# Kernel tuning notes

Hardware: AMD Instinct MI355X
Metric: run time of the kernel (lower is better)

Reference implementation:

```python
import jax, jax.numpy as jnp
import numpy as np

B, C_IN, C_OUT, N, E = 1, 64, 64, 100000, 3200000
BN_EPS = 1e-5


def setup_inputs() -> dict:
    key = jax.random.key(0)
    ks = jax.random.split(key, 8)
    return {
        "in_features": jax.random.normal(ks[0], (B, C_IN, N), dtype=jnp.float32),
        "w_v": jax.random.normal(ks[1], (C_OUT, C_IN), dtype=jnp.float32) * (1.0 / np.sqrt(C_IN)),
        "w_n": jax.random.normal(ks[2], (C_OUT, C_IN), dtype=jnp.float32) * (1.0 / np.sqrt(C_IN)),
        "gamma": jnp.ones((C_OUT,), dtype=jnp.float32),
        "beta": jnp.zeros((C_OUT,), dtype=jnp.float32),
        "prelu_a": jnp.full((1,), 0.25, dtype=jnp.float32),
        "reduce_index": jax.random.randint(ks[3], (E,), 0, N, dtype=jnp.int32),
        "gather_index": jax.random.randint(ks[4], (E,), 0, N, dtype=jnp.int32),
    }


def reference(in_features, w_v, w_n, gamma, beta, prelu_a, reduce_index, gather_index):
    # 1x1 convs == per-node linear maps: [B, C_in, N] -> [B, C_out, N]
    F_v = jnp.einsum('oi,bin->bon', w_v, in_features)
    F_n = jnp.einsum('oi,bin->bon', w_n, in_features)

    # gather source-node features per edge: [E, B, C_out]
    src = jnp.moveaxis(F_n[:, :, gather_index], 2, 0)
    # scatter-mean into destination nodes (include_self=False -> 0 for isolated nodes)
    sums = jax.ops.segment_sum(src, reduce_index, num_segments=N)  # [N, B, C]
    counts = jax.ops.segment_sum(jnp.ones((src.shape[0],), src.dtype), reduce_index,
                                 num_segments=N)  # [N]
    mean = sums / jnp.maximum(counts, 1.0)[:, None, None]  # nodes w/o edges stay 0
    out = jnp.moveaxis(mean, 0, 2) + F_v  # [B, C, N]

    # BatchNorm1d (training mode: biased batch stats over (B, N))
    mu = jnp.mean(out, axis=(0, 2), keepdims=True)
    var = jnp.mean((out - mu) ** 2, axis=(0, 2), keepdims=True)
    out = (out - mu) * jax.lax.rsqrt(var + BN_EPS)
    out = out * gamma[None, :, None] + beta[None, :, None]

    # PReLU with a single shared learnable slope
    out = jnp.where(out >= 0, out, prelu_a[0] * out)
    return out
```

## Files before the change

kernel.cpp:

```cpp
#include <hip/hip_runtime.h>
#include <hip/hip_bf16.h>

#define NODES 100000
#define BN_EPS 1e-5f
#define NB2 256
#define NPB2 391
#define CAP 13072
#define EPB 2048

__device__ __forceinline__ unsigned bf16rne(float f) {
    unsigned u = __float_as_uint(f);
    u += 0x7FFFu + ((u >> 16) & 1u);
    return u >> 16;
}
__device__ __forceinline__ float bflo(unsigned u) { return __uint_as_float(u << 16); }
__device__ __forceinline__ float bfhi(unsigned u) { return __uint_as_float(u & 0xFFFF0000u); }

__global__ __launch_bounds__(256, 8) void k_place(
        const int* __restrict__ ridx, const int* __restrict__ gidx,
        int* __restrict__ cursor, unsigned* __restrict__ packed, int E) {
    __shared__ int lh[4][NB2];
    const int t = threadIdx.x;
    const int w = t >> 6;
    for (int k = t; k < 4 * NB2; k += 256) ((int*)lh)[k] = 0;
    __syncthreads();
    const int base = blockIdx.x * EPB;
    int r[EPB / 256], g[EPB / 256];
#pragma unroll
    for (int k = 0; k < EPB / 256; ++k) {
        int e = base + t + (k << 8);
        r[k] = (e < E) ? ridx[e] : -1;
        g[k] = (e < E) ? gidx[e] : 0;
    }
#pragma unroll
    for (int k = 0; k < EPB / 256; ++k)
        if (r[k] >= 0) atomicAdd(&lh[w][(unsigned)r[k] / NPB2], 1);
    __syncthreads();
    {
        int c0 = lh[0][t], c1 = lh[1][t], c2 = lh[2][t], c3 = lh[3][t];
        int tot = c0 + c1 + c2 + c3;
        if (tot) {
            int g0 = t * CAP + atomicAdd(&cursor[t], tot);
            lh[0][t] = g0;
            lh[1][t] = g0 + c0;
            lh[2][t] = g0 + c0 + c1;
            lh[3][t] = g0 + c0 + c1 + c2;
        }
    }
    __syncthreads();
#pragma unroll
    for (int k = 0; k < EPB / 256; ++k) {
        if (r[k] >= 0) {
            unsigned rr = (unsigned)r[k];
            unsigned b = rr / NPB2;
            int off = atomicAdd(&lh[w][b], 1);
            if (off < (int)((b + 1) * CAP))
                packed[off] = ((rr - b * NPB2) << 17) | (unsigned)g[k];
        }
    }
}

__global__ __launch_bounds__(1024) void k_sortb(
        const int* __restrict__ cursor, unsigned* __restrict__ packed,
        int* __restrict__ nodestart, int* __restrict__ cnt) {
    __shared__ int lh[1024];
    __shared__ int lsc[1024];
    const int b = blockIdx.x, t = threadIdx.x;
    const int s0b = b * CAP;
    int cntb = cursor[b];
    if (cntb > CAP) cntb = CAP;
    unsigned r[(CAP + 1023) / 1024];
#pragma unroll
    for (int kk = 0; kk < (CAP + 1023) / 1024; ++kk) {
        int k = t + kk * 1024;
        if (k < cntb) r[kk] = packed[s0b + k];
    }
    lh[t] = 0;
    __syncthreads();
#pragma unroll
    for (int kk = 0; kk < (CAP + 1023) / 1024; ++kk) {
        int k = t + kk * 1024;
        if (k < cntb) atomicAdd(&lh[r[kk] >> 17], 1);
    }
    __syncthreads();
    lsc[t] = lh[t];
    __syncthreads();
    for (int off = 1; off < 1024; off <<= 1) {
        int v = lsc[t];
        int add = (t >= off) ? lsc[t - off] : 0;
        __syncthreads();
        lsc[t] = v + add;
        __syncthreads();
    }
    int excl = (t == 0) ? 0 : lsc[t - 1];
    if (t < NPB2) {
        int n = b * NPB2 + t;
        if (n < NODES) {
            nodestart[n] = s0b + excl;
            cnt[n] = lh[t];
        }
    }
    __syncthreads();
    lh[t] = excl;
    __syncthreads();
#pragma unroll
    for (int kk = 0; kk < (CAP + 1023) / 1024; ++kk) {
        int k = t + kk * 1024;
        if (k < cntb) {
            unsigned v = r[kk];
            int pos = atomicAdd(&lh[v >> 17], 1);
            packed[s0b + pos] = v & 0x1FFFFu;
        }
    }
}

__global__ __launch_bounds__(256, 4) void k_gemm_bf16(
        const float* __restrict__ x, const float* __restrict__ wn,
        unsigned* __restrict__ Fnh2) {
    __shared__ float lx[64 * 68];
    __shared__ float wt[64 * 68];
    const int t = threadIdx.x;
    const int n0 = blockIdx.x * 64;
    for (int idx = t; idx < 1024; idx += 256) {
        int rr = idx >> 4;
        int q4 = (idx & 15) * 4;
        int n = n0 + q4;
        float4 xv = {0.f, 0.f, 0.f, 0.f};
        if (n < NODES) xv = *(const float4*)(x + rr * NODES + n);
        *(float4*)&lx[rr * 68 + q4] = xv;
        float4 w4 = *(const float4*)(wn + (idx << 2));
        wt[(q4 + 0) * 68 + rr] = w4.x;
        wt[(q4 + 1) * 68 + rr] = w4.y;
        wt[(q4 + 2) * 68 + rr] = w4.z;
        wt[(q4 + 3) * 68 + rr] = w4.w;
    }
    __syncthreads();
    const int c4 = (t & 15) * 4;
    const int j4 = (t >> 4) * 4;
    float4 a0 = {0,0,0,0}, a1 = {0,0,0,0}, a2 = {0,0,0,0}, a3 = {0,0,0,0};
#pragma unroll 8
    for (int ci = 0; ci < 64; ++ci) {
        float4 w = *(const float4*)&wt[ci * 68 + c4];
        float4 xv = *(const float4*)&lx[ci * 68 + j4];
        a0.x += w.x * xv.x; a0.y += w.x * xv.y; a0.z += w.x * xv.z; a0.w += w.x * xv.w;
        a1.x += w.y * xv.x; a1.y += w.y * xv.y; a1.z += w.y * xv.z; a1.w += w.y * xv.w;
        a2.x += w.z * xv.x; a2.y += w.z * xv.y; a2.z += w.z * xv.z; a2.w += w.z * xv.w;
        a3.x += w.w * xv.x; a3.y += w.w * xv.y; a3.z += w.w * xv.z; a3.w += w.w * xv.w;
    }
    uint2* F2 = (uint2*)Fnh2;
#pragma unroll
    for (int k = 0; k < 4; ++k) {
        int n = n0 + j4 + k;
        if (n < NODES) {
            float v0 = (k == 0) ? a0.x : (k == 1) ? a0.y : (k == 2) ? a0.z : a0.w;
            float v1 = (k == 0) ? a1.x : (k == 1) ? a1.y : (k == 2) ? a1.z : a1.w;
            float v2 = (k == 0) ? a2.x : (k == 1) ? a2.y : (k == 2) ? a2.z : a2.w;
            float v3 = (k == 0) ? a3.x : (k == 1) ? a3.y : (k == 2) ? a3.z : a3.w;
            uint2 val;
            val.x = bf16rne(v0) | (bf16rne(v1) << 16);
            val.y = bf16rne(v2) | (bf16rne(v3) << 16);
            F2[n * 16 + (c4 >> 2)] = val;
        }
    }
}

__global__ __launch_bounds__(256) void k_gemm_n(
        const float* __restrict__ x, const float* __restrict__ wn,
        float* __restrict__ Fn) {
    __shared__ float lx[64][65];
    __shared__ float lw[64][65];
    const int t = threadIdx.x;
    const int n0 = blockIdx.x * 64;
    for (int idx = t; idx < 4096; idx += 256) {
        int r = idx >> 6, q = idx & 63;
        lw[r][q] = wn[idx];
        int n = n0 + q;
        lx[r][q] = (n < NODES) ? x[r * NODES + n] : 0.f;
    }
    __syncthreads();
    const int c = t & 63;
    const int jb = t >> 6;
    for (int k = 0; k < 16; ++k) {
        int j = jb + 4 * k;
        int n = n0 + j;
        if (n >= NODES) continue;
        float acc = 0.f;
#pragma unroll
        for (int ci = 0; ci < 64; ++ci)
            acc += lw[c][ci] * lx[ci][j];
        Fn[n * 64 + c] = acc;
    }
}

__global__ __launch_bounds__(256) void k_segreduce(
        const unsigned* __restrict__ Fnh2, const unsigned* __restrict__ packed,
        const int* __restrict__ nodestart, const int* __restrict__ cnt,
        float4* __restrict__ mean4) {
    const int n = (int)((blockIdx.x * 256u + threadIdx.x) >> 6);
    if (n >= NODES) return;
    const int lane = threadIdx.x & 63;
    const int sub = lane >> 3;
    const int cp  = lane & 7;
    const int s0 = nodestart[n];
    const int cn = cnt[n];
    const int s1 = s0 + cn;
    float f0 = 0.f, f1 = 0.f, f2 = 0.f, f3 = 0.f;
    float f4 = 0.f, f5 = 0.f, f6 = 0.f, f7 = 0.f;
    int i = s0;
    for (; i + 15 < s1; i += 16) {
        int ga = (int)packed[i + sub];
        int gb = (int)packed[i + 8 + sub];
        uint4 ua = *(const uint4*)(Fnh2 + (((size_t)ga) << 5) + (cp << 2));
        uint4 ub = *(const uint4*)(Fnh2 + (((size_t)gb) << 5) + (cp << 2));
        f0 += bflo(ua.x) + bflo(ub.x);
        f1 += bfhi(ua.x) + bfhi(ub.x);
        f2 += bflo(ua.y) + bflo(ub.y);
        f3 += bfhi(ua.y) + bfhi(ub.y);
        f4 += bflo(ua.z) + bflo(ub.z);
        f5 += bfhi(ua.z) + bfhi(ub.z);
        f6 += bflo(ua.w) + bflo(ub.w);
        f7 += bfhi(ua.w) + bfhi(ub.w);
    }
    for (; i < s1; i += 8) {
        uint4 u = {0u, 0u, 0u, 0u};
        if (i + sub < s1) {
            int g = (int)packed[i + sub];
            u = *(const uint4*)(Fnh2 + (((size_t)g) << 5) + (cp << 2));
        }
        f0 += bflo(u.x); f1 += bfhi(u.x);
        f2 += bflo(u.y); f3 += bfhi(u.y);
        f4 += bflo(u.z); f5 += bfhi(u.z);
        f6 += bflo(u.w); f7 += bfhi(u.w);
    }
#pragma unroll
    for (int m = 8; m < 64; m <<= 1) {
        f0 += __shfl_xor(f0, m);
        f1 += __shfl_xor(f1, m);
        f2 += __shfl_xor(f2, m);
        f3 += __shfl_xor(f3, m);
        f4 += __shfl_xor(f4, m);
        f5 += __shfl_xor(f5, m);
        f6 += __shfl_xor(f6, m);
        f7 += __shfl_xor(f7, m);
    }
    if (sub == 0) {
        float inv = 1.f / fmaxf((float)cn, 1.f);
        float4 lo4, hi4;
        lo4.x = f0 * inv; lo4.y = f1 * inv; lo4.z = f2 * inv; lo4.w = f3 * inv;
        hi4.x = f4 * inv; hi4.y = f5 * inv; hi4.z = f6 * inv; hi4.w = f7 * inv;
        mean4[n * 16 + cp * 2]     = lo4;
        mean4[n * 16 + cp * 2 + 1] = hi4;
    }
}

__global__ __launch_bounds__(256, 8) void k_combine(
        const float* __restrict__ x, const float* __restrict__ wv,
        const float* __restrict__ sums, const int* __restrict__ counts,
        const int divide,
        float* __restrict__ outpre, float* __restrict__ bn) {
    __shared__ float wt[64 * 68];
    __shared__ float reds[64][5];
    __shared__ float redq[64][5];
    const int t = threadIdx.x;
    const int n0 = blockIdx.x * 64;
    for (int idx = t; idx < 1024; idx += 256) {
        int rr = idx & 63;
        int q4 = (idx >> 6) * 4;
        float4 w4 = *(const float4*)(wv + rr * 64 + q4);
        wt[(q4 + 0) * 68 + rr] = w4.x;
        wt[(q4 + 1) * 68 + rr] = w4.y;
        wt[(q4 + 2) * 68 + rr] = w4.z;
        wt[(q4 + 3) * 68 + rr] = w4.w;
    }
    __syncthreads();
    const int c4 = (t & 15) * 4;
    const int j4 = (t >> 4) * 4;
    const int jn = n0 + j4;
    const bool valid = (jn < NODES);
    const int jc = valid ? jn : 0;
    float4 a0 = {0,0,0,0}, a1 = {0,0,0,0}, a2 = {0,0,0,0}, a3 = {0,0,0,0};
#pragma unroll 4
    for (int ci = 0; ci < 64; ++ci) {
        float4 w = *(const float4*)&wt[ci * 68 + c4];
        float4 xv = *(const float4*)(x + (size_t)ci * NODES + jc);
        a0.x += w.x * xv.x; a0.y += w.x * xv.y; a0.z += w.x * xv.z; a0.w += w.x * xv.w;
        a1.x += w.y * xv.x; a1.y += w.y * xv.y; a1.z += w.y * xv.z; a1.w += w.y * xv.w;
        a2.x += w.z * xv.x; a2.y += w.z * xv.y; a2.z += w.z * xv.z; a2.w += w.z * xv.w;
        a3.x += w.w * xv.x; a3.y += w.w * xv.y; a3.z += w.w * xv.z; a3.w += w.w * xv.w;
    }
    const float4* sums4 = (const float4*)sums;
    float4 mv0 = {0,0,0,0}, mv1 = {0,0,0,0}, mv2 = {0,0,0,0}, mv3 = {0,0,0,0};
    if (valid) {
        mv0 = sums4[(jn + 0) * 16 + (c4 >> 2)];
        mv1 = sums4[(jn + 1) * 16 + (c4 >> 2)];
        mv2 = sums4[(jn + 2) * 16 + (c4 >> 2)];
        mv3 = sums4[(jn + 3) * 16 + (c4 >> 2)];
        if (divide) {
            float i0 = 1.f / fmaxf((float)counts[jn + 0], 1.f);
            float i1 = 1.f / fmaxf((float)counts[jn + 1], 1.f);
            float i2 = 1.f / fmaxf((float)counts[jn + 2], 1.f);
            float i3 = 1.f / fmaxf((float)counts[jn + 3], 1.f);
            mv0.x *= i0; mv0.y *= i0; mv0.z *= i0; mv0.w *= i0;
            mv1.x *= i1; mv1.y *= i1; mv1.z *= i1; mv1.w *= i1;
            mv2.x *= i2; mv2.y *= i2; mv2.z *= i2; mv2.w *= i2;
            mv3.x *= i3; mv3.y *= i3; mv3.z *= i3; mv3.w *= i3;
        }
    }
    float4 st0 = {0,0,0,0}, st1 = {0,0,0,0}, st2 = {0,0,0,0}, st3 = {0,0,0,0};
    if (valid) {
        st0.x = mv0.x + a0.x; st0.y = mv1.x + a0.y; st0.z = mv2.x + a0.z; st0.w = mv3.x + a0.w;
        st1.x = mv0.y + a1.x; st1.y = mv1.y + a1.y; st1.z = mv2.y + a1.z; st1.w = mv3.y + a1.w;
        st2.x = mv0.z + a2.x; st2.y = mv1.z + a2.y; st2.z = mv2.z + a2.z; st2.w = mv3.z + a2.w;
        st3.x = mv0.w + a3.x; st3.y = mv1.w + a3.y; st3.z = mv2.w + a3.z; st3.w = mv3.w + a3.w;
        *(float4*)(outpre + (size_t)(c4 + 0) * NODES + jn) = st0;
        *(float4*)(outpre + (size_t)(c4 + 1) * NODES + jn) = st1;
        *(float4*)(outpre + (size_t)(c4 + 2) * NODES + jn) = st2;
        *(float4*)(outpre + (size_t)(c4 + 3) * NODES + jn) = st3;
    }
    float ls0 = st0.x + st0.y + st0.z + st0.w;
    float ls1 = st1.x + st1.y + st1.z + st1.w;
    float ls2 = st2.x + st2.y + st2.z + st2.w;
    float ls3 = st3.x + st3.y + st3.z + st3.w;
    float lq0 = st0.x*st0.x + st0.y*st0.y + st0.z*st0.z + st0.w*st0.w;
    float lq1 = st1.x*st1.x + st1.y*st1.y + st1.z*st1.z + st1.w*st1.w;
    float lq2 = st2.x*st2.x + st2.y*st2.y + st2.z*st2.z + st2.w*st2.w;
    float lq3 = st3.x*st3.x + st3.y*st3.y + st3.z*st3.z + st3.w*st3.w;
    const int lane = t & 63;
    const int wid = t >> 6;
#pragma unroll
    for (int m = 16; m < 64; m <<= 1) {
        ls0 += __shfl_xor(ls0, m); lq0 += __shfl_xor(lq0, m);
        ls1 += __shfl_xor(ls1, m); lq1 += __shfl_xor(lq1, m);
        ls2 += __shfl_xor(ls2, m); lq2 += __shfl_xor(lq2, m);
        ls3 += __shfl_xor(ls3, m); lq3 += __shfl_xor(lq3, m);
    }
    if (lane < 16) {
        reds[lane * 4 + 0][wid] = ls0; redq[lane * 4 + 0][wid] = lq0;
        reds[lane * 4 + 1][wid] = ls1; redq[lane * 4 + 1][wid] = lq1;
        reds[lane * 4 + 2][wid] = ls2; redq[lane * 4 + 2][wid] = lq2;
        reds[lane * 4 + 3][wid] = ls3; redq[lane * 4 + 3][wid] = lq3;
    }
    __syncthreads();
    if (t < 64) {
        float s = reds[t][0] + reds[t][1] + reds[t][2] + reds[t][3];
        float q = redq[t][0] + redq[t][1] + redq[t][2] + redq[t][3];
        atomicAdd(&bn[t], s);
        atomicAdd(&bn[64 + t], q);
    }
}

__global__ __launch_bounds__(256) void k_final(
        float* __restrict__ out, const float* __restrict__ bn,
        const float* __restrict__ gamma, const float* __restrict__ beta,
        const float* __restrict__ pa) {
    const int c = blockIdx.y;
    const int n = blockIdx.x * 256 + threadIdx.x;
    const float invN = 1.f / (float)NODES;
    float mu = bn[c] * invN;
    float var = fmaxf(bn[64 + c] * invN - mu * mu, 0.f);
    float scale = gamma[c] * rsqrtf(var + BN_EPS);
    float shift = beta[c] - mu * scale;
    float a = pa[0];
    if (n < NODES) {
        float y = out[c * NODES + n] * scale + shift;
        y = (y >= 0.f) ? y : a * y;
        out[c * NODES + n] = y;
    }
}

__global__ __launch_bounds__(256) void k_scatter(
        const float* __restrict__ Fn,
        const int* __restrict__ gidx, const int* __restrict__ ridx,
        float* __restrict__ sums, int* __restrict__ counts, int E) {
    const int wave = (int)((blockIdx.x * blockDim.x + threadIdx.x) >> 6);
    const int lane = threadIdx.x & 63;
    const int base = wave * 64;
    if (base >= E) return;
    const int nvalid = min(64, E - base);
    int g = 0, r = 0;
    if (lane < nvalid) {
        g = gidx[base + lane];
        r = ridx[base + lane];
        atomicAdd(&counts[r], 1);
    }
    for (int i = 0; i < nvalid; ++i) {
        int gg = __shfl(g, i);
        int rr = __shfl(r, i);
        float v = Fn[gg * 64 + lane];
        atomicAdd(&sums[rr * 64 + lane], v);
    }
}

extern "C" void kernel_launch(void* const* d_in, const int* in_sizes, int n_in,
                              void* d_out, int out_size, void* d_ws, size_t ws_size,
                              hipStream_t stream) {
    const float* x     = (const float*)d_in[0];
    const float* w_v   = (const float*)d_in[1];
    const float* w_n   = (const float*)d_in[2];
    const float* gamma = (const float*)d_in[3];
    const float* beta  = (const float*)d_in[4];
    const float* pa    = (const float*)d_in[5];
    const int* ridx    = (const int*)d_in[6];
    const int* gidx    = (const int*)d_in[7];
    float* out = (float*)d_out;

    const int E = in_sizes[6];
    const long long N64 = (long long)NODES * 64;
    const int ntiles = (NODES + 63) / 64;
    const dim3 g4((NODES + 255) / 256, 64);

    size_t need = ((size_t)N64 + (size_t)NB2 * CAP + NB2 + 128
                   + NODES + NODES) * 4;

    if (ws_size >= need) {
        float*    mean      = (float*)d_ws;
        unsigned* packed    = (unsigned*)(mean + N64);
        int*      cursor    = (int*)(packed + (size_t)NB2 * CAP);
        float*    bn        = (float*)(cursor + NB2);
        int*      nodestart = (int*)(bn + 128);
        int*      cntarr    = nodestart + NODES;
        unsigned* Fnh2 = (unsigned*)out;

        hipMemsetAsync(cursor, 0, (NB2 + 128) * sizeof(int), stream);
        k_place<<<(E + EPB - 1) / EPB, 256, 0, stream>>>(ridx, gidx, cursor,
                                                         packed, E);
        k_gemm_bf16<<<ntiles, 256, 0, stream>>>(x, w_n, Fnh2);
        k_sortb<<<NB2, 1024, 0, stream>>>(cursor, packed, nodestart, cntarr);
        k_segreduce<<<(NODES * 64 + 255) / 256, 256, 0, stream>>>(
            Fnh2, packed, nodestart, cntarr, (float4*)mean);
        k_combine<<<ntiles, 256, 0, stream>>>(x, w_v, mean, cntarr, 0, out, bn);
        k_final<<<g4, 256, 0, stream>>>(out, bn, gamma, beta, pa);
    } else {
        float* sums   = (float*)d_ws;
        int*   counts = (int*)(sums + N64);
        float* bn     = (float*)(sums + N64 + NODES);
        float* Fn = out;

        hipMemsetAsync(sums, 0, (size_t)(N64 + NODES + 128) * sizeof(float),
                       stream);
        k_gemm_n<<<ntiles, 256, 0, stream>>>(x, w_n, Fn);
        k_scatter<<<(E + 255) / 256, 256, 0, stream>>>(Fn, gidx, ridx, sums,
                                                       counts, E);
        k_combine<<<ntiles, 256, 0, stream>>>(x, w_v, sums, counts, 1, out, bn);
        k_final<<<g4, 256, 0, stream>>>(out, bn, gamma, beta, pa);
    }
}
```

Measured before the change: 300.5 us.

## Retile node GEMMs over channel blocks and store mean in channel-blocked layout

```diff
diff --git a/kernel.cpp b/kernel.cpp
--- a/kernel.cpp
+++ b/kernel.cpp
@@ -114,52 +114,58 @@
     }
 }
 
-__global__ __launch_bounds__(256, 4) void k_gemm_bf16(
+__global__ __launch_bounds__(256, 3) void k_gemm_bf16_2(
         const float* __restrict__ x, const float* __restrict__ wn,
         unsigned* __restrict__ Fnh2) {
-    __shared__ float lx[64 * 68];
-    __shared__ float wt[64 * 68];
+    __shared__ float wt[64 * 16];
     const int t = threadIdx.x;
-    const int n0 = blockIdx.x * 64;
+    const int cb = blockIdx.y;
+    const int c0 = cb * 16;
     for (int idx = t; idx < 1024; idx += 256) {
-        int rr = idx >> 4;
-        int q4 = (idx & 15) * 4;
-        int n = n0 + q4;
-        float4 xv = {0.f, 0.f, 0.f, 0.f};
-        if (n < NODES) xv = *(const float4*)(x + rr * NODES + n);
-        *(float4*)&lx[rr * 68 + q4] = xv;
-        float4 w4 = *(const float4*)(wn + (idx << 2));
-        wt[(q4 + 0) * 68 + rr] = w4.x;
-        wt[(q4 + 1) * 68 + rr] = w4.y;
-        wt[(q4 + 2) * 68 + rr] = w4.z;
-        wt[(q4 + 3) * 68 + rr] = w4.w;
-    }
-    __syncthreads();
-    const int c4 = (t & 15) * 4;
-    const int j4 = (t >> 4) * 4;
-    float4 a0 = {0,0,0,0}, a1 = {0,0,0,0}, a2 = {0,0,0,0}, a3 = {0,0,0,0};
-#pragma unroll 8
+        int ci = idx >> 4, co = idx & 15;
+        wt[ci * 16 + co] = wn[(c0 + co) * 64 + ci];
+    }
+    __syncthreads();
+    const int j4 = (blockIdx.x * 256 + t) * 4;
+    const bool valid = (j4 < NODES);
+    const int jc = valid ? j4 : 0;
+    float4 acc[16];
+#pragma unroll
+    for (int q = 0; q < 16; ++q) acc[q] = {0.f, 0.f, 0.f, 0.f};
+#pragma unroll 2
     for (int ci = 0; ci < 64; ++ci) {
-        float4 w = *(const float4*)&wt[ci * 68 + c4];
-        float4 xv = *(const float4*)&lx[ci * 68 + j4];
-        a0.x += w.x * xv.x; a0.y += w.x * xv.y; a0.z += w.x * xv.z; a0.w += w.x * xv.w;
-        a1.x += w.y * xv.x; a1.y += w.y * xv.y; a1.z += w.y * xv.z; a1.w += w.y * xv.w;
-        a2.x += w.z * xv.x; a2.y += w.z * xv.y; a2.z += w.z * xv.z; a2.w += w.z * xv.w;
-        a3.x += w.w * xv.x; a3.y += w.w * xv.y; a3.z += w.w * xv.z; a3.w += w.w * xv.w;
-    }
-    uint2* F2 = (uint2*)Fnh2;
-#pragma unroll
-    for (int k = 0; k < 4; ++k) {
-        int n = n0 + j4 + k;
-        if (n < NODES) {
-            float v0 = (k == 0) ? a0.x : (k == 1) ? a0.y : (k == 2) ? a0.z : a0.w;
-            float v1 = (k == 0) ? a1.x : (k == 1) ? a1.y : (k == 2) ? a1.z : a1.w;
-            float v2 = (k == 0) ? a2.x : (k == 1) ? a2.y : (k == 2) ? a2.z : a2.w;
-            float v3 = (k == 0) ? a3.x : (k == 1) ? a3.y : (k == 2) ? a3.z : a3.w;
-            uint2 val;
-            val.x = bf16rne(v0) | (bf16rne(v1) << 16);
-            val.y = bf16rne(v2) | (bf16rne(v3) << 16);
-            F2[n * 16 + (c4 >> 2)] = val;
+        float4 xv = *(const float4*)(x + (size_t)ci * NODES + jc);
+        float wr[16];
+        *(float4*)&wr[0]  = *(const float4*)&wt[ci * 16 + 0];
+        *(float4*)&wr[4]  = *(const float4*)&wt[ci * 16 + 4];
+        *(float4*)&wr[8]  = *(const float4*)&wt[ci * 16 + 8];
+        *(float4*)&wr[12] = *(const float4*)&wt[ci * 16 + 12];
+#pragma unroll
+        for (int q = 0; q < 16; ++q) {
+            acc[q].x += wr[q] * xv.x; acc[q].y += wr[q] * xv.y;
+            acc[q].z += wr[q] * xv.z; acc[q].w += wr[q] * xv.w;
+        }
+    }
+    if (valid) {
+        unsigned* F = Fnh2 + (size_t)j4 * 32 + cb * 8;
+#pragma unroll
+        for (int k = 0; k < 4; ++k) {
+            float v[16];
+#pragma unroll
+            for (int q = 0; q < 16; ++q)
+                v[q] = (k == 0) ? acc[q].x : (k == 1) ? acc[q].y
+                     : (k == 2) ? acc[q].z : acc[q].w;
+            uint4 A, B;
+            A.x = bf16rne(v[0])  | (bf16rne(v[1])  << 16);
+            A.y = bf16rne(v[2])  | (bf16rne(v[3])  << 16);
+            A.z = bf16rne(v[4])  | (bf16rne(v[5])  << 16);
+            A.w = bf16rne(v[6])  | (bf16rne(v[7])  << 16);
+            B.x = bf16rne(v[8])  | (bf16rne(v[9])  << 16);
+            B.y = bf16rne(v[10]) | (bf16rne(v[11]) << 16);
+            B.z = bf16rne(v[12]) | (bf16rne(v[13]) << 16);
+            B.w = bf16rne(v[14]) | (bf16rne(v[15]) << 16);
+            *(uint4*)(F + k * 32)     = A;
+            *(uint4*)(F + k * 32 + 4) = B;
         }
     }
 }
@@ -248,104 +254,89 @@
         float4 lo4, hi4;
         lo4.x = f0 * inv; lo4.y = f1 * inv; lo4.z = f2 * inv; lo4.w = f3 * inv;
         hi4.x = f4 * inv; hi4.y = f5 * inv; hi4.z = f6 * inv; hi4.w = f7 * inv;
-        mean4[n * 16 + cp * 2]     = lo4;
-        mean4[n * 16 + cp * 2 + 1] = hi4;
-    }
-}
-
-__global__ __launch_bounds__(256, 8) void k_combine(
+        const int cb = cp >> 1;
+        const int r0 = (cp & 1) * 2;
+        mean4[((size_t)cb * NODES + n) * 4 + r0]     = lo4;
+        mean4[((size_t)cb * NODES + n) * 4 + r0 + 1] = hi4;
+    }
+}
+
+__global__ __launch_bounds__(256, 3) void k_combine2(
         const float* __restrict__ x, const float* __restrict__ wv,
-        const float* __restrict__ sums, const int* __restrict__ counts,
+        const float* __restrict__ meanv, const int* __restrict__ counts,
         const int divide,
         float* __restrict__ outpre, float* __restrict__ bn) {
-    __shared__ float wt[64 * 68];
-    __shared__ float reds[64][5];
-    __shared__ float redq[64][5];
+    __shared__ float wt[64 * 16];
     const int t = threadIdx.x;
-    const int n0 = blockIdx.x * 64;
+    const int cb = blockIdx.y;
+    const int c0 = cb * 16;
     for (int idx = t; idx < 1024; idx += 256) {
-        int rr = idx & 63;
-        int q4 = (idx >> 6) * 4;
-        float4 w4 = *(const float4*)(wv + rr * 64 + q4);
-        wt[(q4 + 0) * 68 + rr] = w4.x;
-        wt[(q4 + 1) * 68 + rr] = w4.y;
-        wt[(q4 + 2) * 68 + rr] = w4.z;
-        wt[(q4 + 3) * 68 + rr] = w4.w;
-    }
-    __syncthreads();
-    const int c4 = (t & 15) * 4;
-    const int j4 = (t >> 4) * 4;
-    const int jn = n0 + j4;
-    const bool valid = (jn < NODES);
-    const int jc = valid ? jn : 0;
-    float4 a0 = {0,0,0,0}, a1 = {0,0,0,0}, a2 = {0,0,0,0}, a3 = {0,0,0,0};
-#pragma unroll 4
+        int ci = idx >> 4, co = idx & 15;
+        wt[ci * 16 + co] = wv[(c0 + co) * 64 + ci];
+    }
+    __syncthreads();
+    const int j4 = (blockIdx.x * 256 + t) * 4;
+    const bool valid = (j4 < NODES);
+    const int jc = valid ? j4 : 0;
+    float4 acc[16];
+#pragma unroll
+    for (int q = 0; q < 16; ++q) acc[q] = {0.f, 0.f, 0.f, 0.f};
+#pragma unroll 2
     for (int ci = 0; ci < 64; ++ci) {
-        float4 w = *(const float4*)&wt[ci * 68 + c4];
         float4 xv = *(const float4*)(x + (size_t)ci * NODES + jc);
-        a0.x += w.x * xv.x; a0.y += w.x * xv.y; a0.z += w.x * xv.z; a0.w += w.x * xv.w;
-        a1.x += w.y * xv.x; a1.y += w.y * xv.y; a1.z += w.y * xv.z; a1.w += w.y * xv.w;
-        a2.x += w.z * xv.x; a2.y += w.z * xv.y; a2.z += w.z * xv.z; a2.w += w.z * xv.w;
-        a3.x += w.w * xv.x; a3.y += w.w * xv.y; a3.z += w.w * xv.z; a3.w += w.w * xv.w;
-    }
-    const float4* sums4 = (const float4*)sums;
-    float4 mv0 = {0,0,0,0}, mv1 = {0,0,0,0}, mv2 = {0,0,0,0}, mv3 = {0,0,0,0};
+        float wr[16];
+        *(float4*)&wr[0]  = *(const float4*)&wt[ci * 16 + 0];
+        *(float4*)&wr[4]  = *(const float4*)&wt[ci * 16 + 4];
+        *(float4*)&wr[8]  = *(const float4*)&wt[ci * 16 + 8];
+        *(float4*)&wr[12] = *(const float4*)&wt[ci * 16 + 12];
+#pragma unroll
+        for (int q = 0; q < 16; ++q) {
+            acc[q].x += wr[q] * xv.x; acc[q].y += wr[q] * xv.y;
+            acc[q].z += wr[q] * xv.z; acc[q].w += wr[q] * xv.w;
+        }
+    }
+    float s[16], qs[16];
+#pragma unroll
+    for (int q = 0; q < 16; ++q) { s[q] = 0.f; qs[q] = 0.f; }
     if (valid) {
-        mv0 = sums4[(jn + 0) * 16 + (c4 >> 2)];
-        mv1 = sums4[(jn + 1) * 16 + (c4 >> 2)];
-        mv2 = sums4[(jn + 2) * 16 + (c4 >> 2)];
-        mv3 = sums4[(jn + 3) * 16 + (c4 >> 2)];
+        const float* meanB = meanv + (size_t)cb * NODES * 16;
+        float i0 = 1.f, i1 = 1.f, i2 = 1.f, i3 = 1.f;
         if (divide) {
-            float i0 = 1.f / fmaxf((float)counts[jn + 0], 1.f);
-            float i1 = 1.f / fmaxf((float)counts[jn + 1], 1.f);
-            float i2 = 1.f / fmaxf((float)counts[jn + 2], 1.f);
-            float i3 = 1.f / fmaxf((float)counts[jn + 3], 1.f);
-            mv0.x *= i0; mv0.y *= i0; mv0.z *= i0; mv0.w *= i0;
-            mv1.x *= i1; mv1.y *= i1; mv1.z *= i1; mv1.w *= i1;
-            mv2.x *= i2; mv2.y *= i2; mv2.z *= i2; mv2.w *= i2;
-            mv3.x *= i3; mv3.y *= i3; mv3.z *= i3; mv3.w *= i3;
-        }
-    }
-    float4 st0 = {0,0,0,0}, st1 = {0,0,0,0}, st2 = {0,0,0,0}, st3 = {0,0,0,0};
-    if (valid) {
-        st0.x = mv0.x + a0.x; st0.y = mv1.x + a0.y; st0.z = mv2.x + a0.z; st0.w = mv3.x + a0.w;
-        st1.x = mv0.y + a1.x; st1.y = mv1.y + a1.y; st1.z = mv2.y + a1.z; st1.w = mv3.y + a1.w;
-        st2.x = mv0.z + a2.x; st2.y = mv1.z + a2.y; st2.z = mv2.z + a2.z; st2.w = mv3.z + a2.w;
-        st3.x = mv0.w + a3.x; st3.y = mv1.w + a3.y; st3.z = mv2.w + a3.z; st3.w = mv3.w + a3.w;
-        *(float4*)(outpre + (size_t)(c4 + 0) * NODES + jn) = st0;
-        *(float4*)(outpre + (size_t)(c4 + 1) * NODES + jn) = st1;
-        *(float4*)(outpre + (size_t)(c4 + 2) * NODES + jn) = st2;
-        *(float4*)(outpre + (size_t)(c4 + 3) * NODES + jn) = st3;
-    }
-    float ls0 = st0.x + st0.y + st0.z + st0.w;
-    float ls1 = st1.x + st1.y + st1.z + st1.w;
-    float ls2 = st2.x + st2.y + st2.z + st2.w;
-    float ls3 = st3.x + st3.y + st3.z + st3.w;
-    float lq0 = st0.x*st0.x + st0.y*st0.y + st0.z*st0.z + st0.w*st0.w;
-    float lq1 = st1.x*st1.x + st1.y*st1.y + st1.z*st1.z + st1.w*st1.w;
-    float lq2 = st2.x*st2.x + st2.y*st2.y + st2.z*st2.z + st2.w*st2.w;
-    float lq3 = st3.x*st3.x + st3.y*st3.y + st3.z*st3.z + st3.w*st3.w;
-    const int lane = t & 63;
-    const int wid = t >> 6;
-#pragma unroll
-    for (int m = 16; m < 64; m <<= 1) {
-        ls0 += __shfl_xor(ls0, m); lq0 += __shfl_xor(lq0, m);
-        ls1 += __shfl_xor(ls1, m); lq1 += __shfl_xor(lq1, m);
-        ls2 += __shfl_xor(ls2, m); lq2 += __shfl_xor(lq2, m);
-        ls3 += __shfl_xor(ls3, m); lq3 += __shfl_xor(lq3, m);
-    }
-    if (lane < 16) {
-        reds[lane * 4 + 0][wid] = ls0; redq[lane * 4 + 0][wid] = lq0;
-        reds[lane * 4 + 1][wid] = ls1; redq[lane * 4 + 1][wid] = lq1;
-        reds[lane * 4 + 2][wid] = ls2; redq[lane * 4 + 2][wid] = lq2;
-        reds[lane * 4 + 3][wid] = ls3; redq[lane * 4 + 3][wid] = lq3;
-    }
-    __syncthreads();
-    if (t < 64) {
-        float s = reds[t][0] + reds[t][1] + reds[t][2] + reds[t][3];
-        float q = redq[t][0] + redq[t][1] + redq[t][2] + redq[t][3];
-        atomicAdd(&bn[t], s);
-        atomicAdd(&bn[64 + t], q);
+            i0 = 1.f / fmaxf((float)counts[j4 + 0], 1.f);
+            i1 = 1.f / fmaxf((float)counts[j4 + 1], 1.f);
+            i2 = 1.f / fmaxf((float)counts[j4 + 2], 1.f);
+            i3 = 1.f / fmaxf((float)counts[j4 + 3], 1.f);
+        }
+#pragma unroll
+        for (int q = 0; q < 16; ++q) {
+            float m0 = meanB[(size_t)(j4 + 0) * 16 + q] * i0;
+            float m1 = meanB[(size_t)(j4 + 1) * 16 + q] * i1;
+            float m2 = meanB[(size_t)(j4 + 2) * 16 + q] * i2;
+            float m3 = meanB[(size_t)(j4 + 3) * 16 + q] * i3;
+            float4 st;
+            st.x = acc[q].x + m0;
+            st.y = acc[q].y + m1;
+            st.z = acc[q].z + m2;
+            st.w = acc[q].w + m3;
+            *(float4*)(outpre + (size_t)(c0 + q) * NODES + j4) = st;
+            s[q]  = st.x + st.y + st.z + st.w;
+            qs[q] = st.x * st.x + st.y * st.y + st.z * st.z + st.w * st.w;
+        }
+    }
+#pragma unroll
+    for (int m = 1; m < 64; m <<= 1) {
+#pragma unroll
+        for (int q = 0; q < 16; ++q) {
+            s[q]  += __shfl_xor(s[q],  m);
+            qs[q] += __shfl_xor(qs[q], m);
+        }
+    }
+    if ((t & 63) == 0) {
+#pragma unroll
+        for (int q = 0; q < 16; ++q) {
+            atomicAdd(&bn[c0 + q],      s[q]);
+            atomicAdd(&bn[64 + c0 + q], qs[q]);
+        }
     }
 }
 
@@ -383,11 +374,13 @@
         r = ridx[base + lane];
         atomicAdd(&counts[r], 1);
     }
+    const int cb = lane >> 4;
+    const int cl = lane & 15;
     for (int i = 0; i < nvalid; ++i) {
         int gg = __shfl(g, i);
         int rr = __shfl(r, i);
         float v = Fn[gg * 64 + lane];
-        atomicAdd(&sums[rr * 64 + lane], v);
+        atomicAdd(&sums[((size_t)cb * NODES + rr) * 16 + cl], v);
     }
 }
 
@@ -408,6 +401,7 @@
     const long long N64 = (long long)NODES * 64;
     const int ntiles = (NODES + 63) / 64;
     const dim3 g4((NODES + 255) / 256, 64);
+    const dim3 gg((NODES / 4 + 255) / 256, 4);
 
     size_t need = ((size_t)N64 + (size_t)NB2 * CAP + NB2 + 128
                    + NODES + NODES) * 4;
@@ -424,11 +418,11 @@
         hipMemsetAsync(cursor, 0, (NB2 + 128) * sizeof(int), stream);
         k_place<<<(E + EPB - 1) / EPB, 256, 0, stream>>>(ridx, gidx, cursor,
                                                          packed, E);
-        k_gemm_bf16<<<ntiles, 256, 0, stream>>>(x, w_n, Fnh2);
+        k_gemm_bf16_2<<<gg, 256, 0, stream>>>(x, w_n, Fnh2);
         k_sortb<<<NB2, 1024, 0, stream>>>(cursor, packed, nodestart, cntarr);
         k_segreduce<<<(NODES * 64 + 255) / 256, 256, 0, stream>>>(
             Fnh2, packed, nodestart, cntarr, (float4*)mean);
-        k_combine<<<ntiles, 256, 0, stream>>>(x, w_v, mean, cntarr, 0, out, bn);
+        k_combine2<<<gg, 256, 0, stream>>>(x, w_v, mean, cntarr, 0, out, bn);
         k_final<<<g4, 256, 0, stream>>>(out, bn, gamma, beta, pa);
     } else {
         float* sums   = (float*)d_ws;
@@ -441,7 +435,7 @@
         k_gemm_n<<<ntiles, 256, 0, stream>>>(x, w_n, Fn);
         k_scatter<<<(E + 255) / 256, 256, 0, stream>>>(Fn, gidx, ridx, sums,
                                                        counts, E);
-        k_combine<<<ntiles, 256, 0, stream>>>(x, w_v, sums, counts, 1, out, bn);
+        k_combine2<<<gg, 256, 0, stream>>>(x, w_v, sums, counts, 1, out, bn);
         k_final<<<g4, 256, 0, stream>>>(out, bn, gamma, beta, pa);
     }
 }
```

Result: slower. 451.2 us (+50.2%).
